# Kernel tuning notes

Measured on AMD Instinct MI355X. Metric: run time of the kernel, lower is better.

The kernel has to match this reference:

```python
import jax, jax.numpy as jnp
import numpy as np

D_MODEL = 1024
D_STATE = 16
D_CONV = 4
EXPAND = 2
D_INNER = D_MODEL * EXPAND          # 2048
DT_RANK = max(D_MODEL // 16, 1)     # 64
B_SZ = 2
SEQ = 2048


def setup_inputs() -> dict:
    key = jax.random.key(0)
    ks = jax.random.split(key, 8)
    x = jax.random.normal(ks[0], (B_SZ, SEQ, D_MODEL), jnp.float32)
    w_in = jax.random.normal(ks[1], (D_MODEL, 2 * D_INNER), jnp.float32) * 0.02
    w_conv = jax.random.normal(ks[2], (D_INNER, D_CONV), jnp.float32) * 0.2
    b_conv = jnp.zeros((D_INNER,), jnp.float32)
    w_xproj = jax.random.normal(ks[3], (D_INNER, DT_RANK + 2 * D_STATE), jnp.float32) * 0.02
    dt_std = DT_RANK ** -0.5
    w_dt = jax.random.uniform(ks[4], (DT_RANK, D_INNER), jnp.float32, -dt_std, dt_std)
    dt = jnp.exp(jax.random.uniform(ks[5], (D_INNER,), jnp.float32) * (np.log(0.1) - np.log(0.001)) + np.log(0.001))
    b_dt = dt + jnp.log(-jnp.expm1(-dt))  # inverse-softplus init, as in _init_dt_proj
    A_log = jnp.log(jnp.tile(jnp.arange(1, D_STATE + 1, dtype=jnp.float32), (D_INNER, 1)))
    D = jnp.ones((D_INNER,), jnp.float32)
    w_out = jax.random.normal(ks[6], (D_INNER, D_MODEL), jnp.float32) * 0.02
    return dict(x=x, w_in=w_in, w_conv=w_conv, b_conv=b_conv, w_xproj=w_xproj,
                w_dt=w_dt, b_dt=b_dt, A_log=A_log, D=D, w_out=w_out)


def _forward(x, w_in, w_conv, b_conv, w_xproj, w_dt, b_dt, A_log, D, w_out):
    Bb, L, _ = x.shape
    xz = x @ w_in                                  # [B,L,2*d_inner]
    x_ssm, z = jnp.split(xz, 2, axis=-1)           # each [B,L,d_inner]
    # causal depthwise conv1d (pad left d_conv-1, truncate to L)
    xp = jnp.pad(x_ssm, ((0, 0), (D_CONV - 1, 0), (0, 0)))
    conv = sum(xp[:, k:k + L, :] * w_conv[:, k] for k in range(D_CONV)) + b_conv
    x_ssm = jax.nn.silu(conv)
    x_dbc = x_ssm @ w_xproj                        # [B,L,dt_rank+2*d_state]
    dt, Bm, Cm = jnp.split(x_dbc, [DT_RANK, DT_RANK + D_STATE], axis=-1)
    dt = jax.nn.softplus(dt @ w_dt + b_dt)         # [B,L,d_inner]
    A = -jnp.exp(A_log)                            # [d_inner,d_state]
    A_bar = jnp.exp(dt[..., None] * A)             # [B,L,d_inner,d_state]
    x_db = (x_ssm * dt)[..., None] * Bm[:, :, None, :]  # [B,L,d_inner,d_state]

    def step(h, inp):
        Ab, xd, c = inp                            # [B,d,n], [B,d,n], [B,n]
        h = Ab * h + xd
        y = jnp.einsum('bn,bdn->bd', c, h)
        return h, y

    h0 = jnp.zeros((Bb, D_INNER, D_STATE), x.dtype)
    _, ys = jax.lax.scan(step, h0, (A_bar.transpose(1, 0, 2, 3),
                                    x_db.transpose(1, 0, 2, 3),
                                    Cm.transpose(1, 0, 2)))
    y = ys.transpose(1, 0, 2)                      # [B,L,d_inner]
    y = (y + x_ssm * D) * jax.nn.silu(z)
    return y @ w_out                               # [B,L,d_model]


def reference(x, w_in, w_conv, b_conv, w_xproj, w_dt, b_dt, A_log, D, w_out):
    return _forward(x, w_in, w_conv, b_conv, w_xproj, w_dt, b_dt, A_log, D, w_out)
```

## Files before the change

kernel.cpp:

```cpp
#include <hip/hip_runtime.h>
#include <math.h>

#define SEQ    2048
#define BSZ    2
#define DMODEL 1024
#define DINNER 2048
#define DSTATE 16
#define DTRANK 64
#define MTOT   (BSZ*SEQ)
#define NCHUNK 64
#define LC     (SEQ/NCHUNK)
#define BDN    (BSZ*DINNER*DSTATE)
#define KSPLIT 8
#define NXCD   8

using frag8h = __attribute__((ext_vector_type(8))) _Float16;
using f32x4  = __attribute__((ext_vector_type(4))) float;

__device__ __forceinline__ float fast_rcp(float x) { return __builtin_amdgcn_rcpf(x); }

__device__ __forceinline__ unsigned short f16_bits(float x) {
    _Float16 h = (_Float16)x;
    unsigned short u; __builtin_memcpy(&u, &h, 2); return u;
}
__device__ __forceinline__ float f16_val(unsigned short u) {
    _Float16 h; __builtin_memcpy(&h, &u, 2); return (float)h;
}

#define GLL16(SRC, DST) __builtin_amdgcn_global_load_lds( \
    (const __attribute__((address_space(1))) unsigned int*)(const void*)(SRC), \
    (__attribute__((address_space(3))) unsigned int*)(void*)(DST), 16, 0, 0)


__device__ __forceinline__ void stage_half(const unsigned short* __restrict__ G, int g0, int Kp,
                                           int ktile, int half, unsigned short* Lb,
                                           int wave, int lane)
{
    const int k0 = ktile * 64;
    #pragma unroll
    for (int r = 0; r < 2; ++r) {
        const int slot0 = (wave * 2 + r) * 8;
        const int row0  = slot0 + (slot0 & 64) + (half ? 64 : 0);
        const int row   = row0 + (lane >> 3);
        const int c     = (lane & 7) ^ (row & 7);
        const unsigned short* src = G + (size_t)(g0 + row) * Kp + k0 + c * 8;
        unsigned short* dst = Lb + row0 * 64;
        GLL16(src, dst);
    }
}

template<int QM>
__device__ __forceinline__ void dsA_ld(frag8h (&a)[4][2], const unsigned short* Ab,
                                       int wm, int fr, int fq)
{
    #pragma unroll
    for (int i = 0; i < 4; ++i)
        #pragma unroll
        for (int kk = 0; kk < 2; ++kk) {
            const int row = wm + QM * 64 + i * 16 + fr;
            const int c   = kk * 4 + fq;
            a[i][kk] = *(const frag8h*)(Ab + row * 64 + ((c ^ (row & 7)) * 8));
        }
}

template<int QN>
__device__ __forceinline__ void dsB_ld(frag8h (&b)[2][2], const unsigned short* Bb,
                                       int wn, int fr, int fq)
{
    #pragma unroll
    for (int j = 0; j < 2; ++j)
        #pragma unroll
        for (int kk = 0; kk < 2; ++kk) {
            const int row = wn + QN * 32 + j * 16 + fr;
            const int c   = kk * 4 + fq;
            b[j][kk] = *(const frag8h*)(Bb + row * 64 + ((c ^ (row & 7)) * 8));
        }
}

template<int QM, int QN>
__device__ __forceinline__ void mfma_q(f32x4 (&acc)[8][4], const frag8h (&a)[4][2],
                                       const frag8h (&b)[2][2])
{
    __builtin_amdgcn_s_setprio(1);
    #pragma unroll
    for (int i = 0; i < 4; ++i)
        #pragma unroll
        for (int j = 0; j < 2; ++j)
            #pragma unroll
            for (int kk = 0; kk < 2; ++kk)
                acc[QM*4+i][QN*2+j] = __builtin_amdgcn_mfma_f32_16x16x32_f16(
                    a[i][kk], b[j][kk], acc[QM*4+i][QN*2+j], 0, 0, 0);
    __builtin_amdgcn_s_setprio(0);
}

#define PH_BAR1() do { __builtin_amdgcn_s_barrier();                         \
    asm volatile("s_waitcnt lgkmcnt(0)" ::: "memory");                        \
    __builtin_amdgcn_sched_barrier(0); } while (0)
#define PH_BAR2() __builtin_amdgcn_s_barrier()

__global__ __launch_bounds__(512)
void gemm256_f16(const unsigned short* __restrict__ A, const unsigned short* __restrict__ BT,
                 unsigned short* __restrict__ C, int Kp, int Ncols, int NT)
{
    extern __shared__ unsigned short lds[];
    const int tid  = threadIdx.x;
    const int wave = tid >> 6, lane = tid & 63;
    const int fr = lane & 15, fq = lane >> 4;

    const int nwg = gridDim.x * gridDim.y;
    int flat = blockIdx.y * gridDim.x + blockIdx.x;
    {
        const int q = nwg / NXCD, rr = nwg % NXCD;
        const int x = flat % NXCD, o = flat / NXCD;
        flat = (x < rr ? x * (q + 1) : rr * (q + 1) + (x - rr) * q) + o;
    }
    const int m0 = (flat / gridDim.x) * 256;
    const int n0 = (flat % gridDim.x) * 256;

    const int wm = ((wave >> 2) & 1) * 128;
    const int wn = (wave & 3) * 64;

    unsigned short* A0s = lds;
    unsigned short* B0s = lds + 16384;
    unsigned short* A1s = lds + 32768;
    unsigned short* B1s = lds + 32768 + 16384;

    f32x4 acc[8][4];
    #pragma unroll
    for (int i = 0; i < 8; ++i)
        #pragma unroll
        for (int j = 0; j < 4; ++j)
            acc[i][j] = (f32x4){0.f, 0.f, 0.f, 0.f};

    frag8h a[4][2], b0[2][2], b1[2][2];
    const int ntm = NT - 1;

    stage_half(A,  m0, Kp, 0, 0, A0s, wave, lane);
    stage_half(BT, n0, Kp, 0, 0, B0s, wave, lane);
    stage_half(A,  m0, Kp, 0, 1, A0s, wave, lane);
    stage_half(BT, n0, Kp, 0, 1, B0s, wave, lane);
    stage_half(A,  m0, Kp, 1, 0, A1s, wave, lane);
    stage_half(BT, n0, Kp, 1, 0, B1s, wave, lane);
    asm volatile("s_waitcnt vmcnt(4)" ::: "memory");
    __builtin_amdgcn_s_barrier();

    const int niter = NT >> 1;
    for (int it = 0; it < niter; ++it) {
        const int t = 2 * it;
        dsA_ld<0>(a, A0s, wm, fr, fq);
        dsB_ld<0>(b0, B0s, wn, fr, fq);
        stage_half(A,  m0, Kp, (t + 1) & ntm, 1, A1s, wave, lane);
        PH_BAR1();
        mfma_q<0,0>(acc, a, b0);
        PH_BAR2();
        dsB_ld<1>(b1, B0s, wn, fr, fq);
        stage_half(BT, n0, Kp, (t + 1) & ntm, 1, B1s, wave, lane);
        PH_BAR1();
        mfma_q<0,1>(acc, a, b1);
        PH_BAR2();
        dsA_ld<1>(a, A0s, wm, fr, fq);
        stage_half(A,  m0, Kp, (t + 2) & ntm, 0, A0s, wave, lane);
        PH_BAR1();
        mfma_q<1,0>(acc, a, b0);
        PH_BAR2();
        stage_half(BT, n0, Kp, (t + 2) & ntm, 0, B0s, wave, lane);
        asm volatile("s_waitcnt vmcnt(4)" ::: "memory");
        PH_BAR1();
        mfma_q<1,1>(acc, a, b1);
        PH_BAR2();
        dsA_ld<0>(a, A1s, wm, fr, fq);
        dsB_ld<0>(b0, B1s, wn, fr, fq);
        stage_half(A,  m0, Kp, (t + 2) & ntm, 1, A0s, wave, lane);
        PH_BAR1();
        mfma_q<0,0>(acc, a, b0);
        PH_BAR2();
        dsB_ld<1>(b1, B1s, wn, fr, fq);
        stage_half(BT, n0, Kp, (t + 2) & ntm, 1, B0s, wave, lane);
        PH_BAR1();
        mfma_q<0,1>(acc, a, b1);
        PH_BAR2();
        dsA_ld<1>(a, A1s, wm, fr, fq);
        stage_half(A,  m0, Kp, (t + 3) & ntm, 0, A1s, wave, lane);
        PH_BAR1();
        mfma_q<1,0>(acc, a, b0);
        PH_BAR2();
        stage_half(BT, n0, Kp, (t + 3) & ntm, 0, B1s, wave, lane);
        asm volatile("s_waitcnt vmcnt(4)" ::: "memory");
        PH_BAR1();
        mfma_q<1,1>(acc, a, b1);
        PH_BAR2();
    }

    const int crow = (lane >> 4) * 4, ccol = lane & 15;
    #pragma unroll
    for (int i = 0; i < 8; ++i)
        #pragma unroll
        for (int j = 0; j < 4; ++j)
            #pragma unroll
            for (int v = 0; v < 4; ++v) {
                const int row = m0 + wm + i * 16 + crow + v;
                const int col = n0 + wn + j * 16 + ccol;
                C[(size_t)row * Ncols + col] = f16_bits(acc[i][j][v]);
            }
}

template<int OUTF16>
__global__ __launch_bounds__(256)
void gemm_bt_f16(const unsigned short* __restrict__ A, const unsigned short* __restrict__ BT,
                 void* __restrict__ Cout, int Kp, int N, int klen)
{
    __shared__ unsigned short Asm[2][128 * 32];
    __shared__ unsigned short Bsm[2][128 * 32];
    const int tid  = threadIdx.x;
    const int wave = tid >> 6, lane = tid & 63;
    const int m0 = blockIdx.y * 128, n0 = blockIdx.x * 128;
    const int wm = (wave >> 1) * 64, wn = (wave & 1) * 64;
    const int M = gridDim.y * 128;
    const int kbeg = blockIdx.z * klen;

    const int srow = lane >> 2;
    const int sq   = (lane & 3) ^ ((srow >> 1) & 3);
    const int fr = lane & 15;
    const int fq = (lane >> 4) ^ ((fr >> 1) & 3);

    f32x4 acc[4][4];
    #pragma unroll
    for (int i = 0; i < 4; ++i)
        #pragma unroll
        for (int j = 0; j < 4; ++j)
            acc[i][j] = (f32x4){0.f, 0.f, 0.f, 0.f};

    #define OSTAGE(K0, BUF) do {                                                  \
        _Pragma("unroll")                                                         \
        for (int r_ = 0; r_ < 2; ++r_) {                                          \
            const int trow_ = (wave * 2 + r_) * 16 + srow;                        \
            GLL16(A  + (size_t)(m0 + trow_) * Kp + (K0) + sq * 8,                 \
                  Asm[BUF] + (wave * 2 + r_) * 512);                              \
            GLL16(BT + (size_t)(n0 + trow_) * Kp + (K0) + sq * 8,                 \
                  Bsm[BUF] + (wave * 2 + r_) * 512);                              \
        } } while (0)

    const int nsteps = klen >> 5;
    OSTAGE(kbeg, 0);
    for (int s = 0; s < nsteps; ++s) {
        const int buf = s & 1;
        if (s + 1 < nsteps) {
            OSTAGE(kbeg + (s + 1) * 32, buf ^ 1);
            asm volatile("s_waitcnt vmcnt(4)" ::: "memory");
        } else {
            asm volatile("s_waitcnt vmcnt(0)" ::: "memory");
        }
        __builtin_amdgcn_s_barrier();
        frag8h av[4], bv[4];
        #pragma unroll
        for (int i = 0; i < 4; ++i)
            av[i] = *(const frag8h*)(Asm[buf] + (wm + i * 16 + fr) * 32 + fq * 8);
        #pragma unroll
        for (int j = 0; j < 4; ++j)
            bv[j] = *(const frag8h*)(Bsm[buf] + (wn + j * 16 + fr) * 32 + fq * 8);
        #pragma unroll
        for (int i = 0; i < 4; ++i)
            #pragma unroll
            for (int j = 0; j < 4; ++j)
                acc[i][j] = __builtin_amdgcn_mfma_f32_16x16x32_f16(av[i], bv[j], acc[i][j], 0, 0, 0);
        __builtin_amdgcn_s_barrier();
    }
    #undef OSTAGE

    const int crow = (lane >> 4) * 4, ccol = lane & 15;
    if (OUTF16) {
        unsigned short* Cz = (unsigned short*)Cout + (size_t)blockIdx.z * M * N;
        #pragma unroll
        for (int i = 0; i < 4; ++i)
            #pragma unroll
            for (int j = 0; j < 4; ++j)
                #pragma unroll
                for (int v = 0; v < 4; ++v) {
                    const int row = m0 + wm + i * 16 + crow + v;
                    const int col = n0 + wn + j * 16 + ccol;
                    Cz[(size_t)row * N + col] = f16_bits(acc[i][j][v]);
                }
    } else {
        float* Cz = (float*)Cout + (size_t)blockIdx.z * M * N;
        #pragma unroll
        for (int i = 0; i < 4; ++i)
            #pragma unroll
            for (int j = 0; j < 4; ++j)
                #pragma unroll
                for (int v = 0; v < 4; ++v) {
                    const int row = m0 + wm + i * 16 + crow + v;
                    const int col = n0 + wn + j * 16 + ccol;
                    Cz[(size_t)row * N + col] = acc[i][j][v];
                }
    }
}

__device__ __forceinline__ void cvt_bt_body(const float* __restrict__ B,
                                            unsigned short* __restrict__ BTp,
                                            int K, int N, int bk, int bn,
                                            float (*t)[65], int tid)
{
    {
        const int r = tid >> 4, c4 = (tid & 15) * 4;
        #pragma unroll
        for (int p = 0; p < 4; ++p) {
            float4 v = *(const float4*)(B + (size_t)(bk + p * 16 + r) * N + bn + c4);
            t[p * 16 + r][c4 + 0] = v.x;
            t[p * 16 + r][c4 + 1] = v.y;
            t[p * 16 + r][c4 + 2] = v.z;
            t[p * 16 + r][c4 + 3] = v.w;
        }
    }
    __syncthreads();
    const int nl = tid >> 2, kc = (tid & 3) * 16;
    unsigned short h[16];
    #pragma unroll
    for (int i = 0; i < 16; ++i)
        h[i] = f16_bits(t[kc + i][nl]);
    unsigned hw[8];
    #pragma unroll
    for (int j = 0; j < 8; ++j)
        hw[j] = (unsigned)h[2 * j] | ((unsigned)h[2 * j + 1] << 16);
    unsigned short* dst = BTp + (size_t)(bn + nl) * K + bk + kc;
    *(uint4*)(dst)     = make_uint4(hw[0], hw[1], hw[2], hw[3]);
    *(uint4*)(dst + 8) = make_uint4(hw[4], hw[5], hw[6], hw[7]);
}

#define NB_XPK  ((MTOT * DMODEL / 4) / 256)
#define NB_WI   ((DMODEL / 64) * ((2 * DINNER) / 64))
#define NB_WO   ((DINNER / 64) * (DMODEL / 64))

__global__ __launch_bounds__(256)
void pack_all(const float* __restrict__ x, const float* __restrict__ w_in,
              const float* __restrict__ w_out,
              unsigned short* __restrict__ x_pk, unsigned short* __restrict__ wi_pk,
              unsigned short* __restrict__ wo_pk)
{
    __shared__ float t[64][65];
    const int bi = blockIdx.x;
    const int tid = threadIdx.x;
    if (bi < NB_XPK) {
        const int idx = bi * 256 + tid;
        float4 v = ((const float4*)x)[idx];
        ((ushort4*)x_pk)[idx] = make_ushort4(f16_bits(v.x), f16_bits(v.y),
                                             f16_bits(v.z), f16_bits(v.w));
    } else if (bi < NB_XPK + NB_WI) {
        const int tt = bi - NB_XPK;
        cvt_bt_body(w_in, wi_pk, DMODEL, 2 * DINNER,
                    (tt & 15) * 64, (tt >> 4) * 64, t, tid);
    } else {
        const int tt = bi - NB_XPK - NB_WI;
        cvt_bt_body(w_out, wo_pk, DINNER, DMODEL,
                    (tt & 31) * 64, (tt >> 5) * 64, t, tid);
    }
}

__global__ __launch_bounds__(256)
void gemm_dt_f32(const float* __restrict__ A, const float* __restrict__ B,
                 unsigned short* __restrict__ C, const float* __restrict__ bias,
                 int M, int N, int K, int lda, int ldb, int ldc)
{
    __shared__ float As[16][68];
    __shared__ float Bs[16][68];
    const int tid = threadIdx.x;
    const int tx = tid & 15, ty = tid >> 4;
    const int m0 = blockIdx.y * 64, n0 = blockIdx.x * 64;
    const int arow = tid >> 2, acol = (tid & 3) << 2;
    const int brow = tid >> 4, bcol = (tid & 15) << 2;
    float acc[4][4] = {{0.f,0.f,0.f,0.f},{0.f,0.f,0.f,0.f},
                       {0.f,0.f,0.f,0.f},{0.f,0.f,0.f,0.f}};

    for (int k0 = 0; k0 < K; k0 += 16) {
        float4 av = *(const float4*)(A + (size_t)(m0 + arow) * lda + k0 + acol);
        float4 bv = *(const float4*)(B + (size_t)(k0 + brow) * ldb + n0 + bcol);
        __syncthreads();
        As[acol+0][arow] = av.x;
        As[acol+1][arow] = av.y;
        As[acol+2][arow] = av.z;
        As[acol+3][arow] = av.w;
        *(float4*)&Bs[brow][bcol] = bv;
        __syncthreads();
        #pragma unroll
        for (int kk = 0; kk < 16; ++kk) {
            float4 a = *(const float4*)&As[kk][ty << 2];
            float4 b = *(const float4*)&Bs[kk][tx << 2];
            float ar[4] = {a.x, a.y, a.z, a.w};
            float br[4] = {b.x, b.y, b.z, b.w};
            #pragma unroll
            for (int i = 0; i < 4; ++i)
                #pragma unroll
                for (int j = 0; j < 4; ++j)
                    acc[i][j] = fmaf(ar[i], br[j], acc[i][j]);
        }
    }

    const int col = n0 + (tx << 2);
    #pragma unroll
    for (int i = 0; i < 4; ++i) {
        const int row = m0 + (ty << 2) + i;
        unsigned short r[4];
        #pragma unroll
        for (int j = 0; j < 4; ++j) {
            const float xb = acc[i][j] + bias[col + j];
            r[j] = f16_bits(fmaxf(xb, 0.f) + __logf(1.f + __expf(-fabsf(xb))));
        }
        *(ushort4*)(C + (size_t)row * ldc + col) = make_ushort4(r[0], r[1], r[2], r[3]);
    }
}

__global__ __launch_bounds__(256)
void gemm_sk_h(const unsigned short* __restrict__ A, const float* __restrict__ B,
               float* __restrict__ P, int M, int N, int Ktot, int lda, int ldb)
{
    __shared__ float As[16][68];
    __shared__ float Bs[16][68];
    const int tid = threadIdx.x;
    const int tx = tid & 15, ty = tid >> 4;
    const int m0 = blockIdx.y * 64, n0 = blockIdx.x * 64;
    const int z = blockIdx.z;
    const int ks = Ktot / KSPLIT;
    const int kbeg = z * ks, kend = kbeg + ks;
    const int arow = tid >> 2, acol = (tid & 3) << 2;
    const int brow = tid >> 4, bcol = (tid & 15) << 2;
    float acc[4][4] = {{0.f,0.f,0.f,0.f},{0.f,0.f,0.f,0.f},
                       {0.f,0.f,0.f,0.f},{0.f,0.f,0.f,0.f}};

    for (int k0 = kbeg; k0 < kend; k0 += 16) {
        ushort4 ah = *(const ushort4*)(A + (size_t)(m0 + arow) * lda + k0 + acol);
        float4 bv = make_float4(0.f, 0.f, 0.f, 0.f);
        if (n0 + bcol < N)
            bv = *(const float4*)(B + (size_t)(k0 + brow) * ldb + n0 + bcol);
        __syncthreads();
        As[acol+0][arow] = f16_val(ah.x);
        As[acol+1][arow] = f16_val(ah.y);
        As[acol+2][arow] = f16_val(ah.z);
        As[acol+3][arow] = f16_val(ah.w);
        *(float4*)&Bs[brow][bcol] = bv;
        __syncthreads();
        #pragma unroll
        for (int kk = 0; kk < 16; ++kk) {
            float4 a = *(const float4*)&As[kk][ty << 2];
            float4 b = *(const float4*)&Bs[kk][tx << 2];
            float ar[4] = {a.x, a.y, a.z, a.w};
            float br[4] = {b.x, b.y, b.z, b.w};
            #pragma unroll
            for (int i = 0; i < 4; ++i)
                #pragma unroll
                for (int j = 0; j < 4; ++j)
                    acc[i][j] = fmaf(ar[i], br[j], acc[i][j]);
        }
    }

    const int col = n0 + (tx << 2);
    if (col >= N) return;
    float* Pz = P + (size_t)z * M * 96;
    #pragma unroll
    for (int i = 0; i < 4; ++i) {
        const int row = m0 + (ty << 2) + i;
        float4 o; o.x = acc[i][0]; o.y = acc[i][1]; o.z = acc[i][2]; o.w = acc[i][3];
        *(float4*)(Pz + (size_t)row * 96 + col) = o;
    }
}

template<int NS>
__global__ __launch_bounds__(256)
void reduce_add(const float* __restrict__ P, float* __restrict__ C, int total4)
{
    const int i = blockIdx.x * 256 + threadIdx.x;
    if (i >= total4) return;
    float4 s = ((const float4*)P)[i];
    #pragma unroll
    for (int z = 1; z < NS; ++z) {
        float4 v = ((const float4*)P)[(size_t)z * total4 + i];
        s.x += v.x; s.y += v.y; s.z += v.z; s.w += v.w;
    }
    ((float4*)C)[i] = s;
}

__global__ __launch_bounds__(256)
void conv_silu_h4(const unsigned short* __restrict__ xz, const float* __restrict__ wconv,
                  const float* __restrict__ bconv, unsigned short* __restrict__ xc)
{
    const int idx = blockIdx.x * 256 + threadIdx.x;
    const int dq  = idx & (DINNER / 4 - 1);
    const int rg  = idx >> 9;
    const int row0 = rg * 4;
    const int l0   = row0 & (SEQ - 1);
    const int d    = dq * 4;

    float wj[4][4];
    #pragma unroll
    for (int j = 0; j < 4; ++j) {
        const float4 t = *(const float4*)(wconv + (d + j) * 4);
        wj[j][0] = t.x; wj[j][1] = t.y; wj[j][2] = t.z; wj[j][3] = t.w;
    }
    const float4 bc = ((const float4*)bconv)[dq];

    float xr[7][4];
    const unsigned short* xp = xz + (size_t)row0 * (2 * DINNER) + d;
    #pragma unroll
    for (int m = 0; m < 7; ++m) {
        if (l0 + m - 3 >= 0) {
            const ushort4 v = *(const ushort4*)(xp + (ptrdiff_t)(m - 3) * (2 * DINNER));
            xr[m][0] = f16_val(v.x); xr[m][1] = f16_val(v.y);
            xr[m][2] = f16_val(v.z); xr[m][3] = f16_val(v.w);
        } else {
            xr[m][0] = xr[m][1] = xr[m][2] = xr[m][3] = 0.f;
        }
    }

    #pragma unroll
    for (int j = 0; j < 4; ++j) {
        float acc[4] = {bc.x, bc.y, bc.z, bc.w};
        #pragma unroll
        for (int k = 0; k < 4; ++k) {
            acc[0] = fmaf(xr[j + k][0], wj[0][k], acc[0]);
            acc[1] = fmaf(xr[j + k][1], wj[1][k], acc[1]);
            acc[2] = fmaf(xr[j + k][2], wj[2][k], acc[2]);
            acc[3] = fmaf(xr[j + k][3], wj[3][k], acc[3]);
        }
        unsigned short o[4];
        #pragma unroll
        for (int i = 0; i < 4; ++i)
            o[i] = f16_bits(acc[i] * fast_rcp(1.f + __expf(-acc[i])));
        *(ushort4*)(xc + (size_t)(row0 + j) * DINNER + d) = make_ushort4(o[0], o[1], o[2], o[3]);
    }
}


#define EPOW16(q, e) do {                                              \
    const float q2_ = (q)*(q), q4_ = q2_*q2_, q8_ = q4_*q4_;           \
    e[0]=(q);      e[1]=q2_;      e[2]=q2_*(q);  e[3]=q4_;             \
    e[4]=q4_*(q);  e[5]=q4_*q2_;  e[6]=q4_*e[2]; e[7]=q8_;             \
    e[8]=q8_*(q);  e[9]=q8_*q2_;  e[10]=q8_*e[2];e[11]=q8_*q4_;        \
    e[12]=q8_*e[4];e[13]=q8_*e[5];e[14]=q8_*e[6];e[15]=q8_*q8_;        \
} while (0)

__global__ __launch_bounds__(256, 4)
void scan_a_v2(const unsigned short* __restrict__ dtb, const unsigned short* __restrict__ xc,
               const float* __restrict__ dbc,
               float* __restrict__ SH, float* __restrict__ Qp)
{
    __shared__ float bcs[32][32];
    __shared__ unsigned short dtt[2][2048];
    __shared__ unsigned short xct[2][2048];

    const int tid = threadIdx.x;
    const int bi  = blockIdx.x;
    const int c   = bi >> 4;
    const int b   = (bi >> 3) & 1;
    const int d0  = (bi & 7) << 8;
    const int d   = d0 + tid;
    const int r0  = b * SEQ + c * LC;

    const int srow = tid >> 5;
    const int scol = (tid & 31) << 3;
    const size_t sdt = (size_t)(r0 + srow) * DINNER + d0 + scol;

    GLL16(dbc + (size_t)(r0 + (tid >> 3)) * 96 + 64 + (tid & 7) * 4, &bcs[0][0] + tid * 4);
    GLL16(dtb + sdt,                      dtt[0] + tid * 8);
    GLL16(xc  + sdt,                      xct[0] + tid * 8);
    GLL16(dtb + sdt + 8 * DINNER,         dtt[1] + tid * 8);
    GLL16(xc  + sdt + 8 * DINNER,         xct[1] + tid * 8);
    asm volatile("s_waitcnt vmcnt(2)" ::: "memory");
    __builtin_amdgcn_s_barrier();

    float h[16];
    #pragma unroll
    for (int n = 0; n < 16; ++n) h[n] = 0.f;
    float qprod = 1.f;

    for (int g = 0; g < 4; ++g) {
        const int buf = g & 1;
        #pragma unroll
        for (int lg = 0; lg < 8; ++lg) {
            const int l = (g << 3) + lg;
            const float dtv = f16_val(dtt[buf][(lg << 8) + tid]);
            const float xv  = f16_val(xct[buf][(lg << 8) + tid]);
            const float q   = __expf(-dtv);
            qprod *= q;
            const float xd  = xv * dtv;
            float e[16];
            EPOW16(q, e);
            float Bv[16];
            *(float4*)&Bv[0]  = *(const float4*)&bcs[l][0];
            *(float4*)&Bv[4]  = *(const float4*)&bcs[l][4];
            *(float4*)&Bv[8]  = *(const float4*)&bcs[l][8];
            *(float4*)&Bv[12] = *(const float4*)&bcs[l][12];
            #pragma unroll
            for (int n = 0; n < 16; ++n)
                h[n] = fmaf(e[n], h[n], xd * Bv[n]);
        }
        __builtin_amdgcn_s_barrier();
        if (g < 2) {
            GLL16(dtb + sdt + (size_t)(g + 2) * 8 * DINNER, dtt[buf] + tid * 8);
            GLL16(xc  + sdt + (size_t)(g + 2) * 8 * DINNER, xct[buf] + tid * 8);
            asm volatile("s_waitcnt vmcnt(2)" ::: "memory");
        } else {
            asm volatile("s_waitcnt vmcnt(0)" ::: "memory");
        }
        __builtin_amdgcn_s_barrier();
    }

    const size_t off = (size_t)c * BDN + (size_t)b * (DINNER * DSTATE) + (size_t)d * DSTATE;
    *(float4*)(SH + off)      = (float4){h[0],  h[1],  h[2],  h[3]};
    *(float4*)(SH + off + 4)  = (float4){h[4],  h[5],  h[6],  h[7]};
    *(float4*)(SH + off + 8)  = (float4){h[8],  h[9],  h[10], h[11]};
    *(float4*)(SH + off + 12) = (float4){h[12], h[13], h[14], h[15]};
    Qp[(size_t)c * (BSZ * DINNER) + b * DINNER + d] = qprod;
}

__global__ __launch_bounds__(256)
void scan_phase_b(float* __restrict__ SH, const float* __restrict__ Qp)
{
    const int bdn = blockIdx.x * 256 + threadIdx.x;
    const int n = bdn & 15;
    const int d = (bdn >> 4) & (DINNER - 1);
    const int b = bdn >> 15;
    const int m = n + 1;
    float h = 0.f;
    #pragma unroll
    for (int c = 0; c < NCHUNK; ++c) {
        const float s = SH[(size_t)c * BDN + bdn];
        SH[(size_t)c * BDN + bdn] = h;
        const float q = Qp[(size_t)c * (BSZ * DINNER) + b * DINNER + d];
        float r = (m & 1) ? q : 1.f;
        float t = q * q;
        r = (m & 2) ? r * t : r;  t = t * t;
        r = (m & 4) ? r * t : r;  t = t * t;
        r = (m & 8) ? r * t : r;  t = t * t;
        r = (m & 16) ? r * t : r;
        h = r * h + s;
    }
}

__global__ __launch_bounds__(256, 4)
void scan_c_v2(const unsigned short* __restrict__ dtb, const unsigned short* __restrict__ xc,
               const float* __restrict__ dbc, const unsigned short* __restrict__ xz,
               const float* __restrict__ Dvec,
               const float* __restrict__ H, unsigned short* __restrict__ ypk)
{
    __shared__ float bcs[32][32];
    __shared__ unsigned short dtt[2][2048];
    __shared__ unsigned short xct[2][2048];
    __shared__ unsigned short ztt[2][2048];

    const int tid = threadIdx.x;
    const int bi  = blockIdx.x;
    const int c   = bi >> 4;
    const int b   = (bi >> 3) & 1;
    const int d0  = (bi & 7) << 8;
    const int d   = d0 + tid;
    const int r0  = b * SEQ + c * LC;

    const size_t off = (size_t)c * BDN + (size_t)b * (DINNER * DSTATE) + (size_t)d * DSTATE;
    float4 h0 = *(const float4*)(H + off);
    float4 h1 = *(const float4*)(H + off + 4);
    float4 h2 = *(const float4*)(H + off + 8);
    float4 h3 = *(const float4*)(H + off + 12);
    const float Dv = Dvec[d];
    float h[16] = {h0.x, h0.y, h0.z, h0.w, h1.x, h1.y, h1.z, h1.w,
                   h2.x, h2.y, h2.z, h2.w, h3.x, h3.y, h3.z, h3.w};

    const int srow = tid >> 5;
    const int scol = (tid & 31) << 3;
    const size_t sdt = (size_t)(r0 + srow) * DINNER + d0 + scol;
    const size_t sz  = (size_t)(r0 + srow) * (2 * DINNER) + DINNER + d0 + scol;

    GLL16(dbc + (size_t)(r0 + (tid >> 3)) * 96 + 64 + (tid & 7) * 4, &bcs[0][0] + tid * 4);
    GLL16(dtb + sdt,              dtt[0] + tid * 8);
    GLL16(xc  + sdt,              xct[0] + tid * 8);
    GLL16(xz  + sz,               ztt[0] + tid * 8);
    GLL16(dtb + sdt + 8 * DINNER, dtt[1] + tid * 8);
    GLL16(xc  + sdt + 8 * DINNER, xct[1] + tid * 8);
    GLL16(xz  + sz  + 8 * (2 * DINNER), ztt[1] + tid * 8);
    asm volatile("s_waitcnt vmcnt(3)" ::: "memory");
    __builtin_amdgcn_s_barrier();

    for (int g = 0; g < 4; ++g) {
        const int buf = g & 1;
        #pragma unroll
        for (int lg = 0; lg < 8; ++lg) {
            const int l = (g << 3) + lg;
            const float dtv = f16_val(dtt[buf][(lg << 8) + tid]);
            const float xv  = f16_val(xct[buf][(lg << 8) + tid]);
            const float zv  = f16_val(ztt[buf][(lg << 8) + tid]);
            const float q   = __expf(-dtv);
            const float xd  = xv * dtv;
            float e[16];
            EPOW16(q, e);
            float Bv[16], Cv[16];
            *(float4*)&Bv[0]  = *(const float4*)&bcs[l][0];
            *(float4*)&Bv[4]  = *(const float4*)&bcs[l][4];
            *(float4*)&Bv[8]  = *(const float4*)&bcs[l][8];
            *(float4*)&Bv[12] = *(const float4*)&bcs[l][12];
            *(float4*)&Cv[0]  = *(const float4*)&bcs[l][16];
            *(float4*)&Cv[4]  = *(const float4*)&bcs[l][20];
            *(float4*)&Cv[8]  = *(const float4*)&bcs[l][24];
            *(float4*)&Cv[12] = *(const float4*)&bcs[l][28];
            float p0 = 0.f, p1 = 0.f;
            #pragma unroll
            for (int n = 0; n < 16; n += 2) {
                h[n]   = fmaf(e[n],   h[n],   xd * Bv[n]);
                p0     = fmaf(Cv[n],  h[n],   p0);
                h[n+1] = fmaf(e[n+1], h[n+1], xd * Bv[n+1]);
                p1     = fmaf(Cv[n+1],h[n+1], p1);
            }
            const float s = zv * fast_rcp(1.f + __expf(-zv));
            ypk[(size_t)(r0 + l) * DINNER + d] = f16_bits((p0 + p1 + xv * Dv) * s);
        }
        __builtin_amdgcn_s_barrier();
        if (g < 2) {
            GLL16(dtb + sdt + (size_t)(g + 2) * 8 * DINNER,       dtt[buf] + tid * 8);
            GLL16(xc  + sdt + (size_t)(g + 2) * 8 * DINNER,       xct[buf] + tid * 8);
            GLL16(xz  + sz  + (size_t)(g + 2) * 8 * (2 * DINNER), ztt[buf] + tid * 8);
            asm volatile("s_waitcnt vmcnt(11)" ::: "memory");
        } else if (g == 2) {
            asm volatile("s_waitcnt vmcnt(8)" ::: "memory");
        }
        __builtin_amdgcn_s_barrier();
    }
}

extern "C" void kernel_launch(void* const* d_in, const int* in_sizes, int n_in,
                              void* d_out, int out_size, void* d_ws, size_t ws_size,
                              hipStream_t stream)
{
    const float* x      = (const float*)d_in[0];
    const float* w_in   = (const float*)d_in[1];
    const float* w_conv = (const float*)d_in[2];
    const float* b_conv = (const float*)d_in[3];
    const float* w_xproj= (const float*)d_in[4];
    const float* w_dt   = (const float*)d_in[5];
    const float* b_dt   = (const float*)d_in[6];
    const float* Dvec   = (const float*)d_in[8];
    const float* w_out  = (const float*)d_in[9];
    float* out = (float*)d_out;

    char* wsb = (char*)d_ws;
    unsigned short* xz  = (unsigned short*)wsb;
    unsigned short* xc  = xz + (size_t)MTOT * 2 * DINNER;
    unsigned short* dtb = xc + (size_t)MTOT * DINNER;
    float* dbc = (float*)(dtb + (size_t)MTOT * DINNER);
    float* SH  = dbc + (size_t)MTOT * 96;
    float* Qp  = SH  + (size_t)NCHUNK * BDN;
    char*  R1  = (char*)(Qp + (size_t)NCHUNK * BSZ * DINNER);
    unsigned short* wo_pk = (unsigned short*)(R1 + (size_t)MTOT * DINNER * 2);

    unsigned short* x_pk  = (unsigned short*)R1;
    unsigned short* wi_pk = x_pk + (size_t)MTOT * DMODEL;
    unsigned short* ypk   = (unsigned short*)R1;
    float* Psk  = (float*)dtb;

    static bool attr_done = false;
    if (!attr_done) {
        (void)hipFuncSetAttribute((const void*)gemm256_f16,
                                  hipFuncAttributeMaxDynamicSharedMemorySize, 131072);
        attr_done = true;
    }

    pack_all<<<NB_XPK + NB_WI + NB_WO, 256, 0, stream>>>(x, w_in, w_out, x_pk, wi_pk, wo_pk);

    gemm256_f16<<<dim3((2 * DINNER) / 256, MTOT / 256), 512, 131072, stream>>>(
        x_pk, wi_pk, xz, DMODEL, 2 * DINNER, DMODEL / 64);

    conv_silu_h4<<<((MTOT / 4) * (DINNER / 4)) / 256, 256, 0, stream>>>(xz, w_conv, b_conv, xc);

    gemm_sk_h<<<dim3(2, 64, KSPLIT), 256, 0, stream>>>(
        xc, w_xproj, Psk, MTOT, 96, DINNER, DINNER, 96);
    reduce_add<KSPLIT><<<(MTOT * 96 / 4 + 255) / 256, 256, 0, stream>>>(Psk, dbc, MTOT * 96 / 4);

    gemm_dt_f32<<<dim3(32, 64), 256, 0, stream>>>(
        dbc, w_dt, dtb, b_dt, MTOT, DINNER, DTRANK, 96, DINNER, DINNER);

    scan_a_v2<<<1024, 256, 0, stream>>>(dtb, xc, dbc, SH, Qp);
    scan_phase_b<<<BDN / 256, 256, 0, stream>>>(SH, Qp);
    scan_c_v2<<<1024, 256, 0, stream>>>(dtb, xc, dbc, xz, Dvec, SH, ypk);

    gemm_bt_f16<0><<<dim3(DMODEL / 128, MTOT / 128, 1), 256, 0, stream>>>(
        ypk, wo_pk, out, DINNER, DMODEL, DINNER);
}
```

Before: 303.7 us.

## Use 128x64 tiles with triple-buffered prefetch in output projection GEMM

Replaces the output-projection GEMM with a specialized kernel using 128x64 tiles (doubling the grid to 512 blocks) and a three-stage LDS ring buffer that prefetches two K-steps ahead. More blocks should improve CU occupancy on the 4096x1024x2048 GEMM, and the deeper pipeline hides global load latency. The cost is a smaller per-wave tile (2x4 MFMAs), which lowers arithmetic intensity and increases B-matrix reloads.

```diff
diff --git a/kernel.cpp b/kernel.cpp
--- a/kernel.cpp
+++ b/kernel.cpp
@@ -204,95 +204,80 @@
             }
 }
 
-template<int OUTF16>
 __global__ __launch_bounds__(256)
-void gemm_bt_f16(const unsigned short* __restrict__ A, const unsigned short* __restrict__ BT,
-                 void* __restrict__ Cout, int Kp, int N, int klen)
-{
-    __shared__ unsigned short Asm[2][128 * 32];
-    __shared__ unsigned short Bsm[2][128 * 32];
+void gemm_out_f16(const unsigned short* __restrict__ A, const unsigned short* __restrict__ BT,
+                  float* __restrict__ C, int Kp, int N)
+{
+    __shared__ unsigned short Asm[3][128 * 32];
+    __shared__ unsigned short Bsm[3][64 * 32];
     const int tid  = threadIdx.x;
     const int wave = tid >> 6, lane = tid & 63;
-    const int m0 = blockIdx.y * 128, n0 = blockIdx.x * 128;
-    const int wm = (wave >> 1) * 64, wn = (wave & 1) * 64;
-    const int M = gridDim.y * 128;
-    const int kbeg = blockIdx.z * klen;
+    const int m0 = blockIdx.y * 128, n0 = blockIdx.x * 64;
+    const int wm = wave * 32;
 
     const int srow = lane >> 2;
     const int sq   = (lane & 3) ^ ((srow >> 1) & 3);
     const int fr = lane & 15;
     const int fq = (lane >> 4) ^ ((fr >> 1) & 3);
 
-    f32x4 acc[4][4];
-    #pragma unroll
-    for (int i = 0; i < 4; ++i)
+    f32x4 acc[2][4];
+    #pragma unroll
+    for (int i = 0; i < 2; ++i)
         #pragma unroll
         for (int j = 0; j < 4; ++j)
             acc[i][j] = (f32x4){0.f, 0.f, 0.f, 0.f};
 
-    #define OSTAGE(K0, BUF) do {                                                  \
+    #define OSTG(K0, BUF) do {                                                    \
         _Pragma("unroll")                                                         \
         for (int r_ = 0; r_ < 2; ++r_) {                                          \
             const int trow_ = (wave * 2 + r_) * 16 + srow;                        \
-            GLL16(A  + (size_t)(m0 + trow_) * Kp + (K0) + sq * 8,                 \
+            GLL16(A + (size_t)(m0 + trow_) * Kp + (K0) + sq * 8,                  \
                   Asm[BUF] + (wave * 2 + r_) * 512);                              \
-            GLL16(BT + (size_t)(n0 + trow_) * Kp + (K0) + sq * 8,                 \
-                  Bsm[BUF] + (wave * 2 + r_) * 512);                              \
-        } } while (0)
-
-    const int nsteps = klen >> 5;
-    OSTAGE(kbeg, 0);
+        }                                                                         \
+        GLL16(BT + (size_t)(n0 + wave * 16 + srow) * Kp + (K0) + sq * 8,          \
+              Bsm[BUF] + wave * 512);                                             \
+    } while (0)
+
+    const int nsteps = Kp >> 5;
+    OSTG(0, 0);
+    OSTG(32, 1);
+    OSTG(64, 2);
+    int buf = 0;
     for (int s = 0; s < nsteps; ++s) {
-        const int buf = s & 1;
-        if (s + 1 < nsteps) {
-            OSTAGE(kbeg + (s + 1) * 32, buf ^ 1);
-            asm volatile("s_waitcnt vmcnt(4)" ::: "memory");
-        } else {
-            asm volatile("s_waitcnt vmcnt(0)" ::: "memory");
-        }
+        if (s + 2 < nsteps)      asm volatile("s_waitcnt vmcnt(6)" ::: "memory");
+        else if (s + 2 == nsteps) asm volatile("s_waitcnt vmcnt(3)" ::: "memory");
+        else                      asm volatile("s_waitcnt vmcnt(0)" ::: "memory");
         __builtin_amdgcn_s_barrier();
-        frag8h av[4], bv[4];
-        #pragma unroll
-        for (int i = 0; i < 4; ++i)
+        frag8h av[2], bv[4];
+        #pragma unroll
+        for (int i = 0; i < 2; ++i)
             av[i] = *(const frag8h*)(Asm[buf] + (wm + i * 16 + fr) * 32 + fq * 8);
         #pragma unroll
         for (int j = 0; j < 4; ++j)
-            bv[j] = *(const frag8h*)(Bsm[buf] + (wn + j * 16 + fr) * 32 + fq * 8);
-        #pragma unroll
-        for (int i = 0; i < 4; ++i)
+            bv[j] = *(const frag8h*)(Bsm[buf] + (j * 16 + fr) * 32 + fq * 8);
+        #pragma unroll
+        for (int i = 0; i < 2; ++i)
             #pragma unroll
             for (int j = 0; j < 4; ++j)
                 acc[i][j] = __builtin_amdgcn_mfma_f32_16x16x32_f16(av[i], bv[j], acc[i][j], 0, 0, 0);
         __builtin_amdgcn_s_barrier();
-    }
-    #undef OSTAGE
+        if (s + 3 < nsteps)
+            OSTG((s + 3) * 32, buf);
+        buf = (buf == 2) ? 0 : buf + 1;
+    }
+    #undef OSTG
 
     const int crow = (lane >> 4) * 4, ccol = lane & 15;
-    if (OUTF16) {
-        unsigned short* Cz = (unsigned short*)Cout + (size_t)blockIdx.z * M * N;
-        #pragma unroll
-        for (int i = 0; i < 4; ++i)
+    #pragma unroll
+    for (int i = 0; i < 2; ++i)
+        #pragma unroll
+        for (int j = 0; j < 4; ++j)
             #pragma unroll
-            for (int j = 0; j < 4; ++j)
-                #pragma unroll
-                for (int v = 0; v < 4; ++v) {
-                    const int row = m0 + wm + i * 16 + crow + v;
-                    const int col = n0 + wn + j * 16 + ccol;
-                    Cz[(size_t)row * N + col] = f16_bits(acc[i][j][v]);
-                }
-    } else {
-        float* Cz = (float*)Cout + (size_t)blockIdx.z * M * N;
-        #pragma unroll
-        for (int i = 0; i < 4; ++i)
-            #pragma unroll
-            for (int j = 0; j < 4; ++j)
-                #pragma unroll
-                for (int v = 0; v < 4; ++v) {
-                    const int row = m0 + wm + i * 16 + crow + v;
-                    const int col = n0 + wn + j * 16 + ccol;
-                    Cz[(size_t)row * N + col] = acc[i][j][v];
-                }
-    }
+            for (int v = 0; v < 4; ++v) {
+                const int row = m0 + wm + i * 16 + crow + v;
+                const int col = n0 + j * 16 + ccol;
+                C[(size_t)row * N + col] = acc[i][j][v];
+            }
 }
 
 __device__ __forceinline__ void cvt_bt_body(const float* __restrict__ B,
@@ -777,6 +762,6 @@
     scan_phase_b<<<BDN / 256, 256, 0, stream>>>(SH, Qp);
     scan_c_v2<<<1024, 256, 0, stream>>>(dtb, xc, dbc, xz, Dvec, SH, ypk);
 
-    gemm_bt_f16<0><<<dim3(DMODEL / 128, MTOT / 128, 1), 256, 0, stream>>>(
-        ypk, wo_pk, out, DINNER, DMODEL, DINNER);
-}
+    gemm_out_f16<<<dim3(DMODEL / 64, MTOT / 128), 256, 0, stream>>>(
+        ypk, wo_pk, out, DINNER, DMODEL);
+}
```

Result: no change. 305.4 us (+0.6%).
